# Performance work log

Measured on AMD Instinct MI355X. Metric: run time of the kernel, lower is better.

## Reference

```python
import jax, jax.numpy as jnp
import numpy as np

B = 1024
FEATS = [("sirna_gibbs_energy", 19), ("pssm_score", 1), ("gc_sterch", 1), ("sirna_second_percent", 2), ("sirna_second_energy", 2), ("tri_nt_percent", 64), ("di_nt_percent", 16), ("single_nt_percent", 4), ("gc_content", 1)]
DFF = 2048  # torch TransformerEncoderLayer default dim_feedforward


def _posenc(S, d):
    pos = jnp.arange(S, dtype=jnp.float32)[:, None]
    div = jnp.exp(jnp.arange(0, d, 2, dtype=jnp.float32) * (-np.log(10000.0) / d))
    pe = jnp.zeros((S, d), jnp.float32)
    pe = pe.at[:, 0::2].set(jnp.sin(pos * div))
    pe = pe.at[:, 1::2].set(jnp.cos(pos * div))
    return pe


def _ln(x, g, b):
    m = x.mean(-1, keepdims=True)
    v = ((x - m) ** 2).mean(-1, keepdims=True)
    return (x - m) * jax.lax.rsqrt(v + 1e-5) * g + b


def _encoder_layer(x, qkv_w, qkv_b, ow, ob, f1w, f1b, f2w, f2b, g1, b1, g2, b2, nhead):
    Bx, S, d = x.shape
    dh = d // nhead
    qkv = jnp.einsum('bsd,ed->bse', x, qkv_w) + qkv_b  # [B,S,3d]
    q, k, v = jnp.split(qkv, 3, axis=-1)
    sh = lambda t: t.reshape(Bx, S, nhead, dh).transpose(0, 2, 1, 3)  # [B,h,S,dh]
    q, k, v = sh(q), sh(k), sh(v)
    att = jax.nn.softmax(jnp.einsum('bhqd,bhkd->bhqk', q, k) / np.sqrt(dh).astype(np.float32), axis=-1)
    o = jnp.einsum('bhqk,bhkd->bhqd', att, v).transpose(0, 2, 1, 3).reshape(Bx, S, d)
    o = o @ ow.T + ob
    x = _ln(x + o, g1, b1)  # post-norm (norm_first=False default)
    h = jax.nn.relu(x @ f1w.T + f1b) @ f2w.T + f2b
    return _ln(x + h, g2, b2)


def _encoder(x, qkv_w, qkv_b, ow, ob, f1w, f1b, f2w, f2b, g1, b1, g2, b2, nhead):
    for i in range(qkv_w.shape[0]):
        x = _encoder_layer(x, qkv_w[i], qkv_b[i], ow[i], ob[i], f1w[i], f1b[i], f2w[i], f2b[i], g1[i], b1[i], g2[i], b2[i], nhead)
    return x


def setup_inputs():
    key = jax.random.key(0)
    ks = iter(jax.random.split(key, 128))
    inp = {}
    inp['rnafm_encode'] = jax.random.normal(next(ks), (B, 21, 640), jnp.float32)
    inp['rnafm_encode_mrna'] = jax.random.normal(next(ks), (B, 59, 640), jnp.float32)
    for name, n in FEATS:
        inp[name] = jax.random.normal(next(ks), (B, n, 1), jnp.float32)

    def xav(shape):
        fan_out, fan_in = shape[-2], shape[-1]
        std = np.sqrt(2.0 / (fan_in + fan_out)).astype(np.float32)
        return jax.random.normal(next(ks), shape, jnp.float32) * std

    def enc_params(prefix, L, d):
        inp[prefix + '_qkv_w'] = xav((L, 3 * d, d))
        inp[prefix + '_qkv_b'] = jnp.zeros((L, 3 * d), jnp.float32)
        inp[prefix + '_ow'] = xav((L, d, d))
        inp[prefix + '_ob'] = jnp.zeros((L, d), jnp.float32)
        inp[prefix + '_f1w'] = xav((L, DFF, d))
        inp[prefix + '_f1b'] = jnp.zeros((L, DFF), jnp.float32)
        inp[prefix + '_f2w'] = xav((L, d, DFF))
        inp[prefix + '_f2b'] = jnp.zeros((L, d), jnp.float32)
        inp[prefix + '_g1'] = jnp.ones((L, d), jnp.float32)
        inp[prefix + '_b1'] = jnp.zeros((L, d), jnp.float32)
        inp[prefix + '_g2'] = jnp.ones((L, d), jnp.float32)
        inp[prefix + '_b2'] = jnp.zeros((L, d), jnp.float32)

    inp['xmap1_w'] = xav((16, 640)); inp['xmap1_b'] = jnp.zeros(16, jnp.float32)
    enc_params('enc1', 4, 16)
    inp['ymap1_w'] = xav((4, 16)); inp['ymap1_b'] = jnp.zeros(4, jnp.float32)
    inp['xmap2_w'] = xav((8, 640)); inp['xmap2_b'] = jnp.zeros(8, jnp.float32)
    enc_params('enc2', 2, 8)
    inp['ymap2_w'] = xav((1, 8)); inp['ymap2_b'] = jnp.zeros(1, jnp.float32)
    inp['bn_g'] = jnp.ones(253, jnp.float32); inp['bn_b'] = jnp.zeros(253, jnp.float32)
    inp['d1w'] = xav((256, 253)); inp['d1b'] = jnp.zeros(256, jnp.float32)
    inp['d2w'] = xav((64, 256)); inp['d2b'] = jnp.zeros(64, jnp.float32)
    inp['d3w'] = xav((16, 64)); inp['d3b'] = jnp.zeros(16, jnp.float32)
    inp['d4w'] = xav((1, 16)); inp['d4b'] = jnp.zeros(1, jnp.float32)
    return inp


def _forward(rnafm_encode, rnafm_encode_mrna, feats,
             xmap1_w, xmap1_b, enc1, ymap1_w, ymap1_b,
             xmap2_w, xmap2_b, enc2, ymap2_w, ymap2_b,
             bn_g, bn_b, d1w, d1b, d2w, d2b, d3w, d3b, d4w, d4b):
    # siRNA branch: [B,21,640] -> [B,21,16] -> encoder(4 layers, 2 heads) -> [B,21,4]
    x = rnafm_encode @ xmap1_w.T + xmap1_b
    x = x + _posenc(21, 16)
    x = _encoder(x, *enc1, nhead=2)
    as_att = (x @ ymap1_w.T + ymap1_b).reshape(x.shape[0], -1)  # [B,84]
    # mRNA branch: [B,59,640] -> [B,59,8] -> encoder(2 layers, 1 head) -> [B,59,1]
    y = rnafm_encode_mrna @ xmap2_w.T + xmap2_b
    y = y + _posenc(59, 8)
    y = _encoder(y, *enc2, nhead=1)
    mrna_att = (y @ ymap2_w.T + ymap2_b).reshape(y.shape[0], -1)  # [B,59]
    other = jnp.concatenate([f[..., 0] for f in feats], axis=1)  # [B,110]
    cat = jnp.concatenate([as_att, mrna_att, other], axis=1)  # [B,253]
    # BatchNorm1d in eval mode (running_mean=0, running_var=1, eps=1e-5)
    h = cat * jax.lax.rsqrt(jnp.float32(1.0 + 1e-5)) * bn_g + bn_b
    h = jax.nn.leaky_relu(h @ d1w.T + d1b, 0.01)
    h = jax.nn.leaky_relu(h @ d2w.T + d2b, 0.01)
    h = jax.nn.leaky_relu(h @ d3w.T + d3b, 0.01)
    out = jax.nn.sigmoid(h @ d4w.T + d4b)
    return out[:, 0]


def reference(rnafm_encode, rnafm_encode_mrna, sirna_gibbs_energy, pssm_score, gc_sterch,
              sirna_second_percent, sirna_second_energy, tri_nt_percent, di_nt_percent,
              single_nt_percent, gc_content,
              xmap1_w, xmap1_b,
              enc1_qkv_w, enc1_qkv_b, enc1_ow, enc1_ob, enc1_f1w, enc1_f1b, enc1_f2w, enc1_f2b,
              enc1_g1, enc1_b1, enc1_g2, enc1_b2,
              ymap1_w, ymap1_b,
              xmap2_w, xmap2_b,
              enc2_qkv_w, enc2_qkv_b, enc2_ow, enc2_ob, enc2_f1w, enc2_f1b, enc2_f2w, enc2_f2b,
              enc2_g1, enc2_b1, enc2_g2, enc2_b2,
              ymap2_w, ymap2_b,
              bn_g, bn_b, d1w, d1b, d2w, d2b, d3w, d3b, d4w, d4b):
    feats = (sirna_gibbs_energy, pssm_score, gc_sterch, sirna_second_percent,
             sirna_second_energy, tri_nt_percent, di_nt_percent, single_nt_percent, gc_content)
    enc1 = (enc1_qkv_w, enc1_qkv_b, enc1_ow, enc1_ob, enc1_f1w, enc1_f1b, enc1_f2w, enc1_f2b,
            enc1_g1, enc1_b1, enc1_g2, enc1_b2)
    enc2 = (enc2_qkv_w, enc2_qkv_b, enc2_ow, enc2_ob, enc2_f1w, enc2_f1b, enc2_f2w, enc2_f2b,
            enc2_g1, enc2_b1, enc2_g2, enc2_b2)
    return _forward(rnafm_encode, rnafm_encode_mrna, feats,
                    xmap1_w, xmap1_b, enc1, ymap1_w, ymap1_b,
                    xmap2_w, xmap2_b, enc2, ymap2_w, ymap2_b,
                    bn_g, bn_b, d1w, d1b, d2w, d2b, d3w, d3b, d4w, d4b)
```

## Files before the change

kernel.cpp:

```cpp
#include <hip/hip_runtime.h>
#include <math.h>

#define NB 1024

typedef __bf16 mbf8 __attribute__((ext_vector_type(8)));
typedef float  mf4  __attribute__((ext_vector_type(4)));

union Pk { __bf16 h[4]; uint2 u2; };

__device__ __forceinline__ mf4 mfma16(mbf8 a, mbf8 b, mf4 c) {
  return __builtin_amdgcn_mfma_f32_16x16x32_bf16(a, b, c, 0, 0, 0);
}

__device__ __forceinline__ float dot4f(float4 a, float4 b){
  return a.x*b.x + a.y*b.y + a.z*b.z + a.w*b.w;
}

__global__ __launch_bounds__(256) void prep_kernel(
    const float* __restrict__ xw1, const float* __restrict__ f1w1, const float* __restrict__ f2w1,
    const float* __restrict__ xw2, const float* __restrict__ f1w2, const float* __restrict__ f2w2,
    __bf16* __restrict__ out)
{
  int idx = blockIdx.x * 256 + threadIdx.x;
  if (idx >= 610304) return;
  int which, local;
  if (idx < 10240)       { which = 0; local = idx; }
  else if (idx < 272384) { which = 1; local = idx - 10240; }
  else if (idx < 403456) { which = 2; local = idx - 272384; }
  else if (idx < 413696) { which = 3; local = idx - 403456; }
  else if (idx < 544768) { which = 4; local = idx - 413696; }
  else                   { which = 5; local = idx - 544768; }
  int tile = local >> 9, r = local & 511, lane = r >> 3, j = r & 7;
  int quad = lane >> 4, lm = lane & 15, khi = quad * 8 + j;
  float val = 0.f;
  switch (which) {
    case 0: { int k = tile*32 + khi; val = xw1[lm*640 + k]; } break;
    case 1: { int L = tile >> 7, nt = tile & 127, n = nt*16 + lm;
              val = (khi < 16) ? f1w1[(L*2048 + n)*16 + khi] : 0.f; } break;
    case 2: { int L = tile >> 6, ks = tile & 63, k = ks*32 + khi;
              val = f2w1[(L*16 + lm)*2048 + k]; } break;
    case 3: { int k = tile*32 + khi; val = (lm < 8) ? xw2[lm*640 + k] : 0.f; } break;
    case 4: { int L = tile >> 7, nt = tile & 127, n = nt*16 + lm;
              val = (khi < 8) ? f1w2[(L*2048 + n)*8 + khi] : 0.f; } break;
    default:{ int L = tile >> 6, ks = tile & 63, k = ks*32 + khi;
              val = (lm < 8) ? f2w2[(L*8 + lm)*2048 + k] : 0.f; } break;
  }
  out[idx] = (__bf16)val;
}

__global__ __launch_bounds__(256) void b1_kernel(
    const float* __restrict__ inp,
    const float* __restrict__ xb,
    const float* __restrict__ qw, const float* __restrict__ qb,
    const float* __restrict__ ow, const float* __restrict__ ob,
    const float* __restrict__ f1b, const float* __restrict__ f2b,
    const float* __restrict__ g1w, const float* __restrict__ b1w,
    const float* __restrict__ g2w, const float* __restrict__ b2w,
    const float* __restrict__ ymw, const float* __restrict__ ymb,
    const __bf16* __restrict__ xwB, const __bf16* __restrict__ w1B,
    const __bf16* __restrict__ w2B,
    float* __restrict__ outp)
{
  __shared__ __align__(16) float xs[21*20];
  __shared__ __align__(16) float xr[21*20];
  __shared__ __align__(16) float ao[21*20];
  __shared__ __align__(16) float pool[2176];
  __shared__ __align__(16) __bf16 hbuf[32*264];
  __shared__ float mu[21], rsd[21];

  const int tid = threadIdx.x;
  const int b = blockIdx.x;
  const int w = tid >> 6, lane = tid & 63, quad = lane >> 4, lm = lane & 15;
  float* qkv = pool;
  float* sc  = pool + 1092;
  float* red = pool;
  const float* Ain = inp + (size_t)b * 21 * 640;

  mf4 pc0 = {0.f,0.f,0.f,0.f}, pc1 = {0.f,0.f,0.f,0.f};
  for (int i = 0; i < 5; ++i) {
    int ks = w*5 + i;
    mbf8 bv = *(const mbf8*)(xwB + (ks*64 + lane)*8);
    #pragma unroll
    for (int mt = 0; mt < 2; ++mt) {
      int row = mt*16 + lm; row = row > 20 ? 20 : row;
      const float* src = Ain + row*640 + ks*32 + quad*8;
      float4 u0 = *(const float4*)src;
      float4 u1 = *(const float4*)(src + 4);
      mbf8 av;
      av[0]=(__bf16)u0.x; av[1]=(__bf16)u0.y; av[2]=(__bf16)u0.z; av[3]=(__bf16)u0.w;
      av[4]=(__bf16)u1.x; av[5]=(__bf16)u1.y; av[6]=(__bf16)u1.z; av[7]=(__bf16)u1.w;
      if (mt == 0) pc0 = mfma16(av, bv, pc0); else pc1 = mfma16(av, bv, pc1);
    }
  }
  #pragma unroll
  for (int r = 0; r < 4; ++r) {
    red[((w*2+0)*16 + quad*4 + r)*17 + lm] = pc0[r];
    red[((w*2+1)*16 + quad*4 + r)*17 + lm] = pc1[r];
  }
  __syncthreads();
  {
    const float lf = -logf(10000.0f) / 16.0f;
    for (int idx = tid; idx < 336; idx += 256) {
      int t = idx >> 4, i = idx & 15, mt = t >> 4, tl = t & 15;
      float s = red[((0+mt)*16+tl)*17+i] + red[((2+mt)*16+tl)*17+i]
              + red[((4+mt)*16+tl)*17+i] + red[((6+mt)*16+tl)*17+i];
      float freq = expf((float)((i>>1)*2) * lf);
      float pe = (i & 1) ? cosf((float)t * freq) : sinf((float)t * freq);
      xs[t*20 + i] = s + xb[i] + pe;
    }
  }
  __syncthreads();

  for (int L = 0; L < 4; ++L) {
    for (int idx = tid; idx < 1008; idx += 256) {
      int s = idx / 48, e = idx % 48;
      const float* wr = qw + (L*48 + e)*16;
      float a = qb[L*48 + e];
      #pragma unroll
      for (int k = 0; k < 16; ++k) a += xs[s*20+k] * wr[k];
      qkv[s*52 + e] = a;
    }
    __syncthreads();

    for (int idx = tid; idx < 882; idx += 256) {
      int h = idx / 441, r2 = idx % 441, i = r2 / 21, j = r2 % 21;
      float4 q0 = *(const float4*)(qkv + i*52 + h*8);
      float4 q1 = *(const float4*)(qkv + i*52 + h*8 + 4);
      float4 k0 = *(const float4*)(qkv + j*52 + 16 + h*8);
      float4 k1 = *(const float4*)(qkv + j*52 + 16 + h*8 + 4);
      sc[(h*21 + i)*23 + j] = (dot4f(q0,k0) + dot4f(q1,k1)) * 0.35355339059327373f;
    }
    __syncthreads();

    for (int r = tid; r < 42; r += 256) {
      float* row = sc + r*23;
      float m = row[0];
      for (int j = 1; j < 21; ++j) m = fmaxf(m, row[j]);
      float ssum = 0.f;
      for (int j = 0; j < 21; ++j) { float e = __expf(row[j] - m); row[j] = e; ssum += e; }
      float inv = 1.f / ssum;
      for (int j = 0; j < 21; ++j) row[j] *= inv;
    }
    __syncthreads();

    for (int idx = tid; idx < 336; idx += 256) {
      int s = idx >> 4, cc = idx & 15, h = cc >> 3, c = cc & 7;
      const float* row = sc + (h*21 + s)*23;
      float a = 0.f;
      for (int j = 0; j < 21; ++j) a += row[j] * qkv[j*52 + 32 + h*8 + c];
      ao[s*20 + cc] = a;
    }
    __syncthreads();

    for (int idx = tid; idx < 336; idx += 256) {
      int s = idx >> 4, i = idx & 15;
      const float* wr = ow + (L*16 + i)*16;
      float a = ob[L*16 + i];
      #pragma unroll
      for (int c = 0; c < 16; ++c) a += ao[s*20 + c] * wr[c];
      xr[s*20 + i] = xs[s*20 + i] + a;
    }
    __syncthreads();

    if (tid < 21) {
      float m = 0.f;
      #pragma unroll
      for (int k = 0; k < 16; ++k) m += xr[tid*20 + k];
      m *= (1.f/16.f);
      float v = 0.f;
      #pragma unroll
      for (int k = 0; k < 16; ++k) { float d = xr[tid*20 + k] - m; v += d*d; }
      v *= (1.f/16.f);
      mu[tid] = m; rsd[tid] = rsqrtf(v + 1e-5f);
    }
    __syncthreads();
    for (int idx = tid; idx < 336; idx += 256) {
      int s = idx >> 4, i = idx & 15;
      xs[s*20 + i] = (xr[s*20 + i] - mu[s]) * rsd[s] * g1w[L*16+i] + b1w[L*16+i];
    }
    __syncthreads();

    mbf8 xf0, xf1;
    {
      #pragma unroll
      for (int q = 0; q < 8; ++q) { xf0[q] = (__bf16)0.f; xf1[q] = (__bf16)0.f; }
      if (quad < 2) {
        int t0 = lm;
        int t1 = 16 + lm; if (t1 > 20) t1 = 20;
        const float* s0 = xs + t0*20 + quad*8;
        const float* s1 = xs + t1*20 + quad*8;
        float4 a0 = *(const float4*)s0, a1 = *(const float4*)(s0+4);
        float4 b0 = *(const float4*)s1, b1_ = *(const float4*)(s1+4);
        xf0[0]=(__bf16)a0.x; xf0[1]=(__bf16)a0.y; xf0[2]=(__bf16)a0.z; xf0[3]=(__bf16)a0.w;
        xf0[4]=(__bf16)a1.x; xf0[5]=(__bf16)a1.y; xf0[6]=(__bf16)a1.z; xf0[7]=(__bf16)a1.w;
        xf1[0]=(__bf16)b0.x; xf1[1]=(__bf16)b0.y; xf1[2]=(__bf16)b0.z; xf1[3]=(__bf16)b0.w;
        xf1[4]=(__bf16)b1_.x; xf1[5]=(__bf16)b1_.y; xf1[6]=(__bf16)b1_.z; xf1[7]=(__bf16)b1_.w;
      }
    }
    mf4 of0 = {0.f,0.f,0.f,0.f}, of1 = {0.f,0.f,0.f,0.f};
    const __bf16* w1L = w1B + (size_t)L*128*512;
    const __bf16* w2L = w2B + (size_t)L*64*512;
    const float* f1bL = f1b + L*2048;
    for (int ci = 0; ci < 8; ++ci) {
      #pragma unroll
      for (int u = 0; u < 4; ++u) {
        int ut = ci*16 + w*4 + u;
        mbf8 wa = *(const mbf8*)(w1L + (ut*64 + lane)*8);
        float4 bia = *(const float4*)(f1bL + ut*16 + quad*4);
        mf4 z = {0.f,0.f,0.f,0.f};
        mf4 c0 = mfma16(wa, xf0, z);
        mf4 c1 = mfma16(wa, xf1, z);
        Pk p0, p1;
        p0.h[0]=(__bf16)fmaxf(c0[0]+bia.x,0.f); p0.h[1]=(__bf16)fmaxf(c0[1]+bia.y,0.f);
        p0.h[2]=(__bf16)fmaxf(c0[2]+bia.z,0.f); p0.h[3]=(__bf16)fmaxf(c0[3]+bia.w,0.f);
        p1.h[0]=(__bf16)fmaxf(c1[0]+bia.x,0.f); p1.h[1]=(__bf16)fmaxf(c1[1]+bia.y,0.f);
        p1.h[2]=(__bf16)fmaxf(c1[2]+bia.z,0.f); p1.h[3]=(__bf16)fmaxf(c1[3]+bia.w,0.f);
        int colb = (ut & 15)*16 + quad*4;
        *(uint2*)(hbuf + lm*264 + colb)        = p0.u2;
        *(uint2*)(hbuf + (16 + lm)*264 + colb) = p1.u2;
      }
      #pragma unroll
      for (int kk = 0; kk < 2; ++kk) {
        int ksl = w*2 + kk;
        mbf8 wb = *(const mbf8*)(w2L + ((ci*8 + ksl)*64 + lane)*8);
        mbf8 a0 = *(const mbf8*)(hbuf + lm*264 + ksl*32 + quad*8);
        mbf8 a1 = *(const mbf8*)(hbuf + (16 + lm)*264 + ksl*32 + quad*8);
        of0 = mfma16(a0, wb, of0);
        of1 = mfma16(a1, wb, of1);
      }
    }
    __syncthreads();
    #pragma unroll
    for (int r = 0; r < 4; ++r) {
      red[((w*2+0)*16 + quad*4 + r)*17 + lm] = of0[r];
      red[((w*2+1)*16 + quad*4 + r)*17 + lm] = of1[r];
    }
    __syncthreads();
    for (int idx = tid; idx < 336; idx += 256) {
      int t = idx >> 4, i = idx & 15, mt = t >> 4, tl = t & 15;
      float s = red[((0+mt)*16+tl)*17+i] + red[((2+mt)*16+tl)*17+i]
              + red[((4+mt)*16+tl)*17+i] + red[((6+mt)*16+tl)*17+i];
      xr[t*20 + i] = xs[t*20 + i] + s + f2b[L*16 + i];
    }
    __syncthreads();
    if (tid < 21) {
      float m = 0.f;
      #pragma unroll
      for (int k = 0; k < 16; ++k) m += xr[tid*20 + k];
      m *= (1.f/16.f);
      float v = 0.f;
      #pragma unroll
      for (int k = 0; k < 16; ++k) { float d = xr[tid*20 + k] - m; v += d*d; }
      v *= (1.f/16.f);
      mu[tid] = m; rsd[tid] = rsqrtf(v + 1e-5f);
    }
    __syncthreads();
    for (int idx = tid; idx < 336; idx += 256) {
      int s = idx >> 4, i = idx & 15;
      xs[s*20 + i] = (xr[s*20 + i] - mu[s]) * rsd[s] * g2w[L*16+i] + b2w[L*16+i];
    }
    __syncthreads();
  }

  for (int idx = tid; idx < 84; idx += 256) {
    int s = idx >> 2, j = idx & 3;
    float a = ymb[j];
    #pragma unroll
    for (int k = 0; k < 16; ++k) a += xs[s*20 + k] * ymw[j*16 + k];
    outp[(size_t)b*84 + idx] = a;
  }
}

__global__ __launch_bounds__(256) void b2_kernel(
    const float* __restrict__ inp,
    const float* __restrict__ xb,
    const float* __restrict__ qw, const float* __restrict__ qb,
    const float* __restrict__ ow, const float* __restrict__ ob,
    const float* __restrict__ f1b, const float* __restrict__ f2b,
    const float* __restrict__ g1w, const float* __restrict__ b1w,
    const float* __restrict__ g2w, const float* __restrict__ b2w,
    const float* __restrict__ ymw, const float* __restrict__ ymb,
    const __bf16* __restrict__ xwB, const __bf16* __restrict__ w1B,
    const __bf16* __restrict__ w2B,
    float* __restrict__ outp)
{
  __shared__ __align__(16) float xs[59*12];
  __shared__ __align__(16) float xr[59*12];
  __shared__ __align__(16) float ao[59*12];
  __shared__ __align__(16) float pool[5251];
  __shared__ __align__(16) __bf16 hbuf[64*136];
  __shared__ float mu[59], rsd[59];

  const int tid = threadIdx.x;
  const int b = blockIdx.x;
  const int w = tid >> 6, lane = tid & 63, quad = lane >> 4, lm = lane & 15;
  float* qkv = pool;
  float* sc  = pool + 1652;
  float* red = pool;
  const float* Ain = inp + (size_t)b * 59 * 640;

  mf4 pc[4];
  #pragma unroll
  for (int mt = 0; mt < 4; ++mt) { mf4 z = {0.f,0.f,0.f,0.f}; pc[mt] = z; }
  for (int i = 0; i < 5; ++i) {
    int ks = w*5 + i;
    mbf8 bv = *(const mbf8*)(xwB + (ks*64 + lane)*8);
    #pragma unroll
    for (int mt = 0; mt < 4; ++mt) {
      int row = mt*16 + lm; row = row > 58 ? 58 : row;
      const float* src = Ain + row*640 + ks*32 + quad*8;
      float4 u0 = *(const float4*)src;
      float4 u1 = *(const float4*)(src + 4);
      mbf8 av;
      av[0]=(__bf16)u0.x; av[1]=(__bf16)u0.y; av[2]=(__bf16)u0.z; av[3]=(__bf16)u0.w;
      av[4]=(__bf16)u1.x; av[5]=(__bf16)u1.y; av[6]=(__bf16)u1.z; av[7]=(__bf16)u1.w;
      pc[mt] = mfma16(av, bv, pc[mt]);
    }
  }
  #pragma unroll
  for (int mt = 0; mt < 4; ++mt)
    #pragma unroll
    for (int r = 0; r < 4; ++r)
      red[((w*4+mt)*16 + quad*4 + r)*17 + lm] = pc[mt][r];
  __syncthreads();
  {
    const float lf = -logf(10000.0f) / 8.0f;
    for (int idx = tid; idx < 472; idx += 256) {
      int t = idx >> 3, i = idx & 7, mt = t >> 4, tl = t & 15;
      float s = red[((0*4+mt)*16+tl)*17+i] + red[((1*4+mt)*16+tl)*17+i]
              + red[((2*4+mt)*16+tl)*17+i] + red[((3*4+mt)*16+tl)*17+i];
      float freq = expf((float)((i>>1)*2) * lf);
      float pe = (i & 1) ? cosf((float)t * freq) : sinf((float)t * freq);
      xs[t*12 + i] = s + xb[i] + pe;
    }
  }
  __syncthreads();

  for (int L = 0; L < 2; ++L) {
    for (int idx = tid; idx < 1416; idx += 256) {
      int s = idx / 24, e = idx % 24;
      const float* wr = qw + (L*24 + e)*8;
      float a = qb[L*24 + e];
      #pragma unroll
      for (int k = 0; k < 8; ++k) a += xs[s*12+k] * wr[k];
      qkv[s*28 + e] = a;
    }
    __syncthreads();

    for (int idx = tid; idx < 3481; idx += 256) {
      int i = idx / 59, j = idx % 59;
      float4 q0 = *(const float4*)(qkv + i*28);
      float4 q1 = *(const float4*)(qkv + i*28 + 4);
      float4 k0 = *(const float4*)(qkv + j*28 + 8);
      float4 k1 = *(const float4*)(qkv + j*28 + 12);
      sc[i*61 + j] = (dot4f(q0,k0) + dot4f(q1,k1)) * 0.35355339059327373f;
    }
    __syncthreads();

    for (int r = tid; r < 59; r += 256) {
      float* row = sc + r*61;
      float m = row[0];
      for (int j = 1; j < 59; ++j) m = fmaxf(m, row[j]);
      float ssum = 0.f;
      for (int j = 0; j < 59; ++j) { float e = __expf(row[j] - m); row[j] = e; ssum += e; }
      float inv = 1.f / ssum;
      for (int j = 0; j < 59; ++j) row[j] *= inv;
    }
    __syncthreads();

    for (int idx = tid; idx < 472; idx += 256) {
      int s = idx >> 3, c = idx & 7;
      const float* row = sc + s*61;
      float a = 0.f;
      for (int j = 0; j < 59; ++j) a += row[j] * qkv[j*28 + 16 + c];
      ao[s*12 + c] = a;
    }
    __syncthreads();

    for (int idx = tid; idx < 472; idx += 256) {
      int s = idx >> 3, i = idx & 7;
      const float* wr = ow + (L*8 + i)*8;
      float a = ob[L*8 + i];
      #pragma unroll
      for (int c = 0; c < 8; ++c) a += ao[s*12 + c] * wr[c];
      xr[s*12 + i] = xs[s*12 + i] + a;
    }
    __syncthreads();

    if (tid < 59) {
      float m = 0.f;
      #pragma unroll
      for (int k = 0; k < 8; ++k) m += xr[tid*12 + k];
      m *= 0.125f;
      float v = 0.f;
      #pragma unroll
      for (int k = 0; k < 8; ++k) { float d = xr[tid*12 + k] - m; v += d*d; }
      v *= 0.125f;
      mu[tid] = m; rsd[tid] = rsqrtf(v + 1e-5f);
    }
    __syncthreads();
    for (int idx = tid; idx < 472; idx += 256) {
      int s = idx >> 3, i = idx & 7;
      xs[s*12 + i] = (xr[s*12 + i] - mu[s]) * rsd[s] * g1w[L*8+i] + b1w[L*8+i];
    }
    __syncthreads();

    mbf8 xf[4];
    #pragma unroll
    for (int tt = 0; tt < 4; ++tt) {
      #pragma unroll
      for (int q = 0; q < 8; ++q) xf[tt][q] = (__bf16)0.f;
      if (quad == 0) {
        int tok = tt*16 + lm; if (tok > 58) tok = 58;
        const float* src = xs + tok*12;
        float4 u0 = *(const float4*)src, u1 = *(const float4*)(src + 4);
        xf[tt][0]=(__bf16)u0.x; xf[tt][1]=(__bf16)u0.y; xf[tt][2]=(__bf16)u0.z; xf[tt][3]=(__bf16)u0.w;
        xf[tt][4]=(__bf16)u1.x; xf[tt][5]=(__bf16)u1.y; xf[tt][6]=(__bf16)u1.z; xf[tt][7]=(__bf16)u1.w;
      }
    }
    mf4 of[4];
    #pragma unroll
    for (int mt = 0; mt < 4; ++mt) { mf4 z = {0.f,0.f,0.f,0.f}; of[mt] = z; }
    const __bf16* w1L = w1B + (size_t)L*128*512;
    const __bf16* w2L = w2B + (size_t)L*64*512;
    const float* f1bL = f1b + L*2048;
    for (int ci = 0; ci < 16; ++ci) {
      #pragma unroll
      for (int u = 0; u < 2; ++u) {
        int ut = ci*8 + w*2 + u;
        mbf8 wa = *(const mbf8*)(w1L + (ut*64 + lane)*8);
        float4 bia = *(const float4*)(f1bL + ut*16 + quad*4);
        int colb = (ut & 7)*16 + quad*4;
        #pragma unroll
        for (int tt = 0; tt < 4; ++tt) {
          mf4 z = {0.f,0.f,0.f,0.f};
          mf4 c = mfma16(wa, xf[tt], z);
          Pk p;
          p.h[0]=(__bf16)fmaxf(c[0]+bia.x,0.f); p.h[1]=(__bf16)fmaxf(c[1]+bia.y,0.f);
          p.h[2]=(__bf16)fmaxf(c[2]+bia.z,0.f); p.h[3]=(__bf16)fmaxf(c[3]+bia.w,0.f);
          *(uint2*)(hbuf + (tt*16 + lm)*136 + colb) = p.u2;
        }
      }
      {
        mbf8 wb = *(const mbf8*)(w2L + ((ci*4 + w)*64 + lane)*8);
        #pragma unroll
        for (int mt = 0; mt < 4; ++mt) {
          mbf8 ah = *(const mbf8*)(hbuf + (mt*16 + lm)*136 + w*32 + quad*8);
          of[mt] = mfma16(ah, wb, of[mt]);
        }
      }
    }
    __syncthreads();
    #pragma unroll
    for (int mt = 0; mt < 4; ++mt)
      #pragma unroll
      for (int r = 0; r < 4; ++r)
        red[((w*4+mt)*16 + quad*4 + r)*17 + lm] = of[mt][r];
    __syncthreads();
    for (int idx = tid; idx < 472; idx += 256) {
      int t = idx >> 3, i = idx & 7, mt = t >> 4, tl = t & 15;
      float s = red[((0*4+mt)*16+tl)*17+i] + red[((1*4+mt)*16+tl)*17+i]
              + red[((2*4+mt)*16+tl)*17+i] + red[((3*4+mt)*16+tl)*17+i];
      xr[t*12 + i] = xs[t*12 + i] + s + f2b[L*8 + i];
    }
    __syncthreads();
    if (tid < 59) {
      float m = 0.f;
      #pragma unroll
      for (int k = 0; k < 8; ++k) m += xr[tid*12 + k];
      m *= 0.125f;
      float v = 0.f;
      #pragma unroll
      for (int k = 0; k < 8; ++k) { float d = xr[tid*12 + k] - m; v += d*d; }
      v *= 0.125f;
      mu[tid] = m; rsd[tid] = rsqrtf(v + 1e-5f);
    }
    __syncthreads();
    for (int idx = tid; idx < 472; idx += 256) {
      int s = idx >> 3, i = idx & 7;
      xs[s*12 + i] = (xr[s*12 + i] - mu[s]) * rsd[s] * g2w[L*8+i] + b2w[L*8+i];
    }
    __syncthreads();
  }

  for (int s = tid; s < 59; s += 256) {
    float a = ymb[0];
    #pragma unroll
    for (int k = 0; k < 8; ++k) a += xs[s*12 + k] * ymw[k];
    outp[(size_t)b*59 + s] = a;
  }
}

__global__ __launch_bounds__(256) void mlp_kernel(
    const float* __restrict__ as_att, const float* __restrict__ mrna,
    const float* __restrict__ f_gibbs, const float* __restrict__ f_pssm,
    const float* __restrict__ f_gcs, const float* __restrict__ f_ssp,
    const float* __restrict__ f_sse, const float* __restrict__ f_tri,
    const float* __restrict__ f_di, const float* __restrict__ f_sgl,
    const float* __restrict__ f_gc,
    const float* __restrict__ bn_g, const float* __restrict__ bn_b,
    const float* __restrict__ d1w, const float* __restrict__ d1b,
    const float* __restrict__ d2w, const float* __restrict__ d2b,
    const float* __restrict__ d3w, const float* __restrict__ d3b,
    const float* __restrict__ d4w, const float* __restrict__ d4b,
    float* __restrict__ outp)
{
  __shared__ float cat[256];
  __shared__ float l1[256];
  __shared__ float l2[64];
  __shared__ float l3[16];
  const int tid = threadIdx.x;
  const int b   = blockIdx.x;
  const float bnscale = rsqrtf(1.0f + 1e-5f);

  if (tid < 253) {
    float v;
    if (tid < 84)       v = as_att[(size_t)b*84 + tid];
    else if (tid < 143) v = mrna[(size_t)b*59 + (tid - 84)];
    else {
      int j = tid - 143;
      if (j < 19)       v = f_gibbs[b*19 + j];
      else if (j < 20)  v = f_pssm[b];
      else if (j < 21)  v = f_gcs[b];
      else if (j < 23)  v = f_ssp[b*2 + (j-21)];
      else if (j < 25)  v = f_sse[b*2 + (j-23)];
      else if (j < 89)  v = f_tri[b*64 + (j-25)];
      else if (j < 105) v = f_di[b*16 + (j-89)];
      else if (j < 109) v = f_sgl[b*4 + (j-105)];
      else              v = f_gc[b];
    }
    cat[tid] = v * bnscale * bn_g[tid] + bn_b[tid];
  }
  __syncthreads();

  {
    float a = d1b[tid];
    const float* w = d1w + (size_t)tid * 253;
    for (int j = 0; j < 253; ++j) a += cat[j] * w[j];
    l1[tid] = (a > 0.f) ? a : 0.01f * a;
  }
  __syncthreads();
  if (tid < 64) {
    float a = d2b[tid];
    const float* w = d2w + (size_t)tid * 256;
    for (int j = 0; j < 256; ++j) a += l1[j] * w[j];
    l2[tid] = (a > 0.f) ? a : 0.01f * a;
  }
  __syncthreads();
  if (tid < 16) {
    float a = d3b[tid];
    const float* w = d3w + tid * 64;
    for (int j = 0; j < 64; ++j) a += l2[j] * w[j];
    l3[tid] = (a > 0.f) ? a : 0.01f * a;
  }
  __syncthreads();
  if (tid == 0) {
    float a = d4b[0];
    #pragma unroll
    for (int j = 0; j < 16; ++j) a += l3[j] * d4w[j];
    outp[b] = 1.f / (1.f + __expf(-a));
  }
}

extern "C" void kernel_launch(void* const* d_in, const int* in_sizes, int n_in,
                              void* d_out, int out_size, void* d_ws, size_t ws_size,
                              hipStream_t stream) {
  const float* rnafm   = (const float*)d_in[0];
  const float* rnafm_m = (const float*)d_in[1];
  const float* f_gibbs = (const float*)d_in[2];
  const float* f_pssm  = (const float*)d_in[3];
  const float* f_gcs   = (const float*)d_in[4];
  const float* f_ssp   = (const float*)d_in[5];
  const float* f_sse   = (const float*)d_in[6];
  const float* f_tri   = (const float*)d_in[7];
  const float* f_di    = (const float*)d_in[8];
  const float* f_sgl   = (const float*)d_in[9];
  const float* f_gc    = (const float*)d_in[10];
  const float* xmap1_w = (const float*)d_in[11];
  const float* xmap1_b = (const float*)d_in[12];
  const float* e1_qw   = (const float*)d_in[13];
  const float* e1_qb   = (const float*)d_in[14];
  const float* e1_ow   = (const float*)d_in[15];
  const float* e1_ob   = (const float*)d_in[16];
  const float* e1_f1w  = (const float*)d_in[17];
  const float* e1_f1b  = (const float*)d_in[18];
  const float* e1_f2w  = (const float*)d_in[19];
  const float* e1_f2b  = (const float*)d_in[20];
  const float* e1_g1   = (const float*)d_in[21];
  const float* e1_b1   = (const float*)d_in[22];
  const float* e1_g2   = (const float*)d_in[23];
  const float* e1_b2   = (const float*)d_in[24];
  const float* ymap1_w = (const float*)d_in[25];
  const float* ymap1_b = (const float*)d_in[26];
  const float* xmap2_w = (const float*)d_in[27];
  const float* xmap2_b = (const float*)d_in[28];
  const float* e2_qw   = (const float*)d_in[29];
  const float* e2_qb   = (const float*)d_in[30];
  const float* e2_ow   = (const float*)d_in[31];
  const float* e2_ob   = (const float*)d_in[32];
  const float* e2_f1w  = (const float*)d_in[33];
  const float* e2_f1b  = (const float*)d_in[34];
  const float* e2_f2w  = (const float*)d_in[35];
  const float* e2_f2b  = (const float*)d_in[36];
  const float* e2_g1   = (const float*)d_in[37];
  const float* e2_b1   = (const float*)d_in[38];
  const float* e2_g2   = (const float*)d_in[39];
  const float* e2_b2   = (const float*)d_in[40];
  const float* ymap2_w = (const float*)d_in[41];
  const float* ymap2_b = (const float*)d_in[42];
  const float* bn_g    = (const float*)d_in[43];
  const float* bn_b    = (const float*)d_in[44];
  const float* d1w     = (const float*)d_in[45];
  const float* d1b     = (const float*)d_in[46];
  const float* d2w     = (const float*)d_in[47];
  const float* d2b     = (const float*)d_in[48];
  const float* d3w     = (const float*)d_in[49];
  const float* d3b     = (const float*)d_in[50];
  const float* d4w     = (const float*)d_in[51];
  const float* d4b     = (const float*)d_in[52];

  float* as_att = (float*)d_ws;
  float* mrna   = (float*)((char*)d_ws + (size_t)NB*84*4);
  __bf16* bfb   = (__bf16*)((char*)d_ws + 585728);
  __bf16* xw1B  = bfb;
  __bf16* w1B1  = bfb + 10240;
  __bf16* w2B1  = bfb + 272384;
  __bf16* xw2B  = bfb + 403456;
  __bf16* w1B2  = bfb + 413696;
  __bf16* w2B2  = bfb + 544768;
  float* outp   = (float*)d_out;

  prep_kernel<<<2384, 256, 0, stream>>>(xmap1_w, e1_f1w, e1_f2w, xmap2_w, e2_f1w, e2_f2w, bfb);

  b1_kernel<<<NB, 256, 0, stream>>>(rnafm, xmap1_b,
      e1_qw, e1_qb, e1_ow, e1_ob, e1_f1b, e1_f2b,
      e1_g1, e1_b1, e1_g2, e1_b2, ymap1_w, ymap1_b,
      xw1B, w1B1, w2B1, as_att);

  b2_kernel<<<NB, 256, 0, stream>>>(rnafm_m, xmap2_b,
      e2_qw, e2_qb, e2_ow, e2_ob, e2_f1b, e2_f2b,
      e2_g1, e2_b1, e2_g2, e2_b2, ymap2_w, ymap2_b,
      xw2B, w1B2, w2B2, mrna);

  mlp_kernel<<<NB, 256, 0, stream>>>(as_att, mrna,
      f_gibbs, f_pssm, f_gcs, f_ssp, f_sse, f_tri, f_di, f_sgl, f_gc,
      bn_g, bn_b, d1w, d1b, d2w, d2b, d3w, d3b, d4w, d4b, outp);
}
```

Baseline: 573.9 us.

## Batch MLP head on MFMA, alias hbuf into pool, parallelize softmax

The MLP head now processes 16 samples per block and runs its three dense layers with bf16 MFMA instructions. The weights for those layers are converted by the prep kernel into fragment layout, replacing the per-sample scalar fp32 dot products. The encoder kernels alias the FFN hidden buffer into the shared pool to cut LDS use and pad its row stride. Softmax rows are now split across 4 lanes with shuffle reductions instead of one thread per row. This adds bf16 rounding in the MLP head, and the head launches only 64 blocks, which limits its parallelism.

```diff
diff --git a/kernel.cpp b/kernel.cpp
--- a/kernel.cpp
+++ b/kernel.cpp
@@ -16,20 +16,33 @@
   return a.x*b.x + a.y*b.y + a.z*b.z + a.w*b.w;
 }
 
+__device__ __forceinline__ mbf8 ld_frag_f32(const float* p) {
+  float4 u0 = *(const float4*)p;
+  float4 u1 = *(const float4*)(p + 4);
+  mbf8 v;
+  v[0]=(__bf16)u0.x; v[1]=(__bf16)u0.y; v[2]=(__bf16)u0.z; v[3]=(__bf16)u0.w;
+  v[4]=(__bf16)u1.x; v[5]=(__bf16)u1.y; v[6]=(__bf16)u1.z; v[7]=(__bf16)u1.w;
+  return v;
+}
+
 __global__ __launch_bounds__(256) void prep_kernel(
     const float* __restrict__ xw1, const float* __restrict__ f1w1, const float* __restrict__ f2w1,
     const float* __restrict__ xw2, const float* __restrict__ f1w2, const float* __restrict__ f2w2,
+    const float* __restrict__ d1w, const float* __restrict__ d2w, const float* __restrict__ d3w,
     __bf16* __restrict__ out)
 {
   int idx = blockIdx.x * 256 + threadIdx.x;
-  if (idx >= 610304) return;
+  if (idx >= 693248) return;
   int which, local;
   if (idx < 10240)       { which = 0; local = idx; }
   else if (idx < 272384) { which = 1; local = idx - 10240; }
   else if (idx < 403456) { which = 2; local = idx - 272384; }
   else if (idx < 413696) { which = 3; local = idx - 403456; }
   else if (idx < 544768) { which = 4; local = idx - 413696; }
-  else                   { which = 5; local = idx - 544768; }
+  else if (idx < 610304) { which = 5; local = idx - 544768; }
+  else if (idx < 675840) { which = 6; local = idx - 610304; }
+  else if (idx < 692224) { which = 7; local = idx - 675840; }
+  else                   { which = 8; local = idx - 692224; }
   int tile = local >> 9, r = local & 511, lane = r >> 3, j = r & 7;
   int quad = lane >> 4, lm = lane & 15, khi = quad * 8 + j;
   float val = 0.f;
@@ -42,8 +55,14 @@
     case 3: { int k = tile*32 + khi; val = (lm < 8) ? xw2[lm*640 + k] : 0.f; } break;
     case 4: { int L = tile >> 7, nt = tile & 127, n = nt*16 + lm;
               val = (khi < 8) ? f1w2[(L*2048 + n)*8 + khi] : 0.f; } break;
-    default:{ int L = tile >> 6, ks = tile & 63, k = ks*32 + khi;
+    case 5: { int L = tile >> 6, ks = tile & 63, k = ks*32 + khi;
               val = (lm < 8) ? f2w2[(L*8 + lm)*2048 + k] : 0.f; } break;
+    case 6: { int nt = tile >> 3, ks = tile & 7, k = ks*32 + khi;
+              val = (k < 253) ? d1w[(nt*16 + lm)*253 + k] : 0.f; } break;
+    case 7: { int nt = tile >> 3, ks = tile & 7, k = ks*32 + khi;
+              val = d2w[(nt*16 + lm)*256 + k]; } break;
+    default:{ int ks = tile, k = ks*32 + khi;
+              val = d3w[lm*64 + k]; } break;
   }
   out[idx] = (__bf16)val;
 }
@@ -64,8 +83,7 @@
   __shared__ __align__(16) float xs[21*20];
   __shared__ __align__(16) float xr[21*20];
   __shared__ __align__(16) float ao[21*20];
-  __shared__ __align__(16) float pool[2176];
-  __shared__ __align__(16) __bf16 hbuf[32*264];
+  __shared__ __align__(16) float pool[4288];
   __shared__ float mu[21], rsd[21];
 
   const int tid = threadIdx.x;
@@ -74,6 +92,7 @@
   float* qkv = pool;
   float* sc  = pool + 1092;
   float* red = pool;
+  __bf16* hbuf = (__bf16*)pool;
   const float* Ain = inp + (size_t)b * 21 * 640;
 
   mf4 pc0 = {0.f,0.f,0.f,0.f}, pc1 = {0.f,0.f,0.f,0.f};
@@ -83,12 +102,7 @@
     #pragma unroll
     for (int mt = 0; mt < 2; ++mt) {
       int row = mt*16 + lm; row = row > 20 ? 20 : row;
-      const float* src = Ain + row*640 + ks*32 + quad*8;
-      float4 u0 = *(const float4*)src;
-      float4 u1 = *(const float4*)(src + 4);
-      mbf8 av;
-      av[0]=(__bf16)u0.x; av[1]=(__bf16)u0.y; av[2]=(__bf16)u0.z; av[3]=(__bf16)u0.w;
-      av[4]=(__bf16)u1.x; av[5]=(__bf16)u1.y; av[6]=(__bf16)u1.z; av[7]=(__bf16)u1.w;
+      mbf8 av = ld_frag_f32(Ain + row*640 + ks*32 + quad*8);
       if (mt == 0) pc0 = mfma16(av, bv, pc0); else pc1 = mfma16(av, bv, pc1);
     }
   }
@@ -132,14 +146,21 @@
     }
     __syncthreads();
 
-    for (int r = tid; r < 42; r += 256) {
-      float* row = sc + r*23;
-      float m = row[0];
-      for (int j = 1; j < 21; ++j) m = fmaxf(m, row[j]);
-      float ssum = 0.f;
-      for (int j = 0; j < 21; ++j) { float e = __expf(row[j] - m); row[j] = e; ssum += e; }
-      float inv = 1.f / ssum;
-      for (int j = 0; j < 21; ++j) row[j] *= inv;
+    {
+      int r = tid >> 2, p = tid & 3;
+      if (r < 42) {
+        float* row = sc + r*23;
+        float m = -1e30f;
+        for (int j = p; j < 21; j += 4) m = fmaxf(m, row[j]);
+        m = fmaxf(m, __shfl_xor(m, 1));
+        m = fmaxf(m, __shfl_xor(m, 2));
+        float ssum = 0.f;
+        for (int j = p; j < 21; j += 4) { float e = __expf(row[j] - m); row[j] = e; ssum += e; }
+        ssum += __shfl_xor(ssum, 1);
+        ssum += __shfl_xor(ssum, 2);
+        float inv = 1.f / ssum;
+        for (int j = p; j < 21; j += 4) row[j] *= inv;
+      }
     }
     __syncthreads();
 
@@ -187,14 +208,8 @@
       if (quad < 2) {
         int t0 = lm;
         int t1 = 16 + lm; if (t1 > 20) t1 = 20;
-        const float* s0 = xs + t0*20 + quad*8;
-        const float* s1 = xs + t1*20 + quad*8;
-        float4 a0 = *(const float4*)s0, a1 = *(const float4*)(s0+4);
-        float4 b0 = *(const float4*)s1, b1_ = *(const float4*)(s1+4);
-        xf0[0]=(__bf16)a0.x; xf0[1]=(__bf16)a0.y; xf0[2]=(__bf16)a0.z; xf0[3]=(__bf16)a0.w;
-        xf0[4]=(__bf16)a1.x; xf0[5]=(__bf16)a1.y; xf0[6]=(__bf16)a1.z; xf0[7]=(__bf16)a1.w;
-        xf1[0]=(__bf16)b0.x; xf1[1]=(__bf16)b0.y; xf1[2]=(__bf16)b0.z; xf1[3]=(__bf16)b0.w;
-        xf1[4]=(__bf16)b1_.x; xf1[5]=(__bf16)b1_.y; xf1[6]=(__bf16)b1_.z; xf1[7]=(__bf16)b1_.w;
+        xf0 = ld_frag_f32(xs + t0*20 + quad*8);
+        xf1 = ld_frag_f32(xs + t1*20 + quad*8);
       }
     }
     mf4 of0 = {0.f,0.f,0.f,0.f}, of1 = {0.f,0.f,0.f,0.f};
@@ -216,15 +231,15 @@
         p1.h[0]=(__bf16)fmaxf(c1[0]+bia.x,0.f); p1.h[1]=(__bf16)fmaxf(c1[1]+bia.y,0.f);
         p1.h[2]=(__bf16)fmaxf(c1[2]+bia.z,0.f); p1.h[3]=(__bf16)fmaxf(c1[3]+bia.w,0.f);
         int colb = (ut & 15)*16 + quad*4;
-        *(uint2*)(hbuf + lm*264 + colb)        = p0.u2;
-        *(uint2*)(hbuf + (16 + lm)*264 + colb) = p1.u2;
+        *(uint2*)(hbuf + lm*268 + colb)        = p0.u2;
+        *(uint2*)(hbuf + (16 + lm)*268 + colb) = p1.u2;
       }
       #pragma unroll
       for (int kk = 0; kk < 2; ++kk) {
         int ksl = w*2 + kk;
         mbf8 wb = *(const mbf8*)(w2L + ((ci*8 + ksl)*64 + lane)*8);
-        mbf8 a0 = *(const mbf8*)(hbuf + lm*264 + ksl*32 + quad*8);
-        mbf8 a1 = *(const mbf8*)(hbuf + (16 + lm)*264 + ksl*32 + quad*8);
+        mbf8 a0 = *(const mbf8*)(hbuf + lm*268 + ksl*32 + quad*8);
+        mbf8 a1 = *(const mbf8*)(hbuf + (16 + lm)*268 + ksl*32 + quad*8);
         of0 = mfma16(a0, wb, of0);
         of1 = mfma16(a1, wb, of1);
       }
@@ -288,7 +303,6 @@
   __shared__ __align__(16) float xr[59*12];
   __shared__ __align__(16) float ao[59*12];
   __shared__ __align__(16) float pool[5251];
-  __shared__ __align__(16) __bf16 hbuf[64*136];
   __shared__ float mu[59], rsd[59];
 
   const int tid = threadIdx.x;
@@ -297,6 +311,7 @@
   float* qkv = pool;
   float* sc  = pool + 1652;
   float* red = pool;
+  __bf16* hbuf = (__bf16*)pool;
   const float* Ain = inp + (size_t)b * 59 * 640;
 
   mf4 pc[4];
@@ -308,12 +323,7 @@
     #pragma unroll
     for (int mt = 0; mt < 4; ++mt) {
       int row = mt*16 + lm; row = row > 58 ? 58 : row;
-      const float* src = Ain + row*640 + ks*32 + quad*8;
-      float4 u0 = *(const float4*)src;
-      float4 u1 = *(const float4*)(src + 4);
-      mbf8 av;
-      av[0]=(__bf16)u0.x; av[1]=(__bf16)u0.y; av[2]=(__bf16)u0.z; av[3]=(__bf16)u0.w;
-      av[4]=(__bf16)u1.x; av[5]=(__bf16)u1.y; av[6]=(__bf16)u1.z; av[7]=(__bf16)u1.w;
+      mbf8 av = ld_frag_f32(Ain + row*640 + ks*32 + quad*8);
       pc[mt] = mfma16(av, bv, pc[mt]);
     }
   }
@@ -357,14 +367,21 @@
     }
     __syncthreads();
 
-    for (int r = tid; r < 59; r += 256) {
-      float* row = sc + r*61;
-      float m = row[0];
-      for (int j = 1; j < 59; ++j) m = fmaxf(m, row[j]);
-      float ssum = 0.f;
-      for (int j = 0; j < 59; ++j) { float e = __expf(row[j] - m); row[j] = e; ssum += e; }
-      float inv = 1.f / ssum;
-      for (int j = 0; j < 59; ++j) row[j] *= inv;
+    {
+      int r = tid >> 2, p = tid & 3;
+      if (r < 59) {
+        float* row = sc + r*61;
+        float m = -1e30f;
+        for (int j = p; j < 59; j += 4) m = fmaxf(m, row[j]);
+        m = fmaxf(m, __shfl_xor(m, 1));
+        m = fmaxf(m, __shfl_xor(m, 2));
+        float ssum = 0.f;
+        for (int j = p; j < 59; j += 4) { float e = __expf(row[j] - m); row[j] = e; ssum += e; }
+        ssum += __shfl_xor(ssum, 1);
+        ssum += __shfl_xor(ssum, 2);
+        float inv = 1.f / ssum;
+        for (int j = p; j < 59; j += 4) row[j] *= inv;
+      }
     }
     __syncthreads();
 
@@ -412,10 +429,7 @@
       for (int q = 0; q < 8; ++q) xf[tt][q] = (__bf16)0.f;
       if (quad == 0) {
         int tok = tt*16 + lm; if (tok > 58) tok = 58;
-        const float* src = xs + tok*12;
-        float4 u0 = *(const float4*)src, u1 = *(const float4*)(src + 4);
-        xf[tt][0]=(__bf16)u0.x; xf[tt][1]=(__bf16)u0.y; xf[tt][2]=(__bf16)u0.z; xf[tt][3]=(__bf16)u0.w;
-        xf[tt][4]=(__bf16)u1.x; xf[tt][5]=(__bf16)u1.y; xf[tt][6]=(__bf16)u1.z; xf[tt][7]=(__bf16)u1.w;
+        xf[tt] = ld_frag_f32(xs + tok*12);
       }
     }
     mf4 of[4];
@@ -438,14 +452,14 @@
           Pk p;
           p.h[0]=(__bf16)fmaxf(c[0]+bia.x,0.f); p.h[1]=(__bf16)fmaxf(c[1]+bia.y,0.f);
           p.h[2]=(__bf16)fmaxf(c[2]+bia.z,0.f); p.h[3]=(__bf16)fmaxf(c[3]+bia.w,0.f);
-          *(uint2*)(hbuf + (tt*16 + lm)*136 + colb) = p.u2;
+          *(uint2*)(hbuf + (tt*16 + lm)*140 + colb) = p.u2;
         }
       }
       {
         mbf8 wb = *(const mbf8*)(w2L + ((ci*4 + w)*64 + lane)*8);
         #pragma unroll
         for (int mt = 0; mt < 4; ++mt) {
-          mbf8 ah = *(const mbf8*)(hbuf + (mt*16 + lm)*136 + w*32 + quad*8);
+          mbf8 ah = *(const mbf8*)(hbuf + (mt*16 + lm)*140 + w*32 + quad*8);
           of[mt] = mfma16(ah, wb, of[mt]);
         }
       }
@@ -499,66 +513,111 @@
     const float* __restrict__ f_di, const float* __restrict__ f_sgl,
     const float* __restrict__ f_gc,
     const float* __restrict__ bn_g, const float* __restrict__ bn_b,
-    const float* __restrict__ d1w, const float* __restrict__ d1b,
-    const float* __restrict__ d2w, const float* __restrict__ d2b,
-    const float* __restrict__ d3w, const float* __restrict__ d3b,
+    const float* __restrict__ d1b, const float* __restrict__ d2b,
+    const float* __restrict__ d3b,
     const float* __restrict__ d4w, const float* __restrict__ d4b,
+    const __bf16* __restrict__ d1B, const __bf16* __restrict__ d2B,
+    const __bf16* __restrict__ d3B,
     float* __restrict__ outp)
 {
-  __shared__ float cat[256];
-  __shared__ float l1[256];
-  __shared__ float l2[64];
-  __shared__ float l3[16];
+  __shared__ __align__(16) float cat[16*268];
+  __shared__ __align__(16) float h1[16*268];
+  __shared__ __align__(16) float h2[16*68];
+  __shared__ __align__(16) float h3[16*17];
   const int tid = threadIdx.x;
-  const int b   = blockIdx.x;
+  const int bs  = blockIdx.x * 16;
+  const int w = tid >> 6, lane = tid & 63, quad = lane >> 4, lm = lane & 15;
   const float bnscale = rsqrtf(1.0f + 1e-5f);
 
-  if (tid < 253) {
-    float v;
-    if (tid < 84)       v = as_att[(size_t)b*84 + tid];
-    else if (tid < 143) v = mrna[(size_t)b*59 + (tid - 84)];
-    else {
-      int j = tid - 143;
-      if (j < 19)       v = f_gibbs[b*19 + j];
-      else if (j < 20)  v = f_pssm[b];
-      else if (j < 21)  v = f_gcs[b];
-      else if (j < 23)  v = f_ssp[b*2 + (j-21)];
-      else if (j < 25)  v = f_sse[b*2 + (j-23)];
-      else if (j < 89)  v = f_tri[b*64 + (j-25)];
-      else if (j < 105) v = f_di[b*16 + (j-89)];
-      else if (j < 109) v = f_sgl[b*4 + (j-105)];
-      else              v = f_gc[b];
-    }
-    cat[tid] = v * bnscale * bn_g[tid] + bn_b[tid];
-  }
+  for (int g = 0; g < 16; ++g) {
+    int smp = bs + g;
+    for (int j = tid; j < 253; j += 256) {
+      float v;
+      if (j < 84)       v = as_att[(size_t)smp*84 + j];
+      else if (j < 143) v = mrna[(size_t)smp*59 + (j - 84)];
+      else {
+        int j2 = j - 143;
+        if (j2 < 19)       v = f_gibbs[smp*19 + j2];
+        else if (j2 < 20)  v = f_pssm[smp];
+        else if (j2 < 21)  v = f_gcs[smp];
+        else if (j2 < 23)  v = f_ssp[smp*2 + (j2-21)];
+        else if (j2 < 25)  v = f_sse[smp*2 + (j2-23)];
+        else if (j2 < 89)  v = f_tri[smp*64 + (j2-25)];
+        else if (j2 < 105) v = f_di[smp*16 + (j2-89)];
+        else if (j2 < 109) v = f_sgl[smp*4 + (j2-105)];
+        else               v = f_gc[smp];
+      }
+      cat[g*268 + j] = v * bnscale * bn_g[j] + bn_b[j];
+    }
+  }
+  if (tid < 48) { int g = tid / 3; cat[g*268 + 253 + tid % 3] = 0.f; }
   __syncthreads();
 
   {
-    float a = d1b[tid];
-    const float* w = d1w + (size_t)tid * 253;
-    for (int j = 0; j < 253; ++j) a += cat[j] * w[j];
-    l1[tid] = (a > 0.f) ? a : 0.01f * a;
+    mf4 acc[4];
+    #pragma unroll
+    for (int q = 0; q < 4; ++q) { mf4 z = {0.f,0.f,0.f,0.f}; acc[q] = z; }
+    for (int ks = 0; ks < 8; ++ks) {
+      mbf8 af = ld_frag_f32(cat + lm*268 + ks*32 + quad*8);
+      #pragma unroll
+      for (int nt4 = 0; nt4 < 4; ++nt4) {
+        int nt = w*4 + nt4;
+        mbf8 bf = *(const mbf8*)(d1B + ((nt*8 + ks)*64 + lane)*8);
+        acc[nt4] = mfma16(af, bf, acc[nt4]);
+      }
+    }
+    #pragma unroll
+    for (int nt4 = 0; nt4 < 4; ++nt4) {
+      int n = (w*4 + nt4)*16 + lm;
+      float bb = d1b[n];
+      #pragma unroll
+      for (int r = 0; r < 4; ++r) {
+        float a = acc[nt4][r] + bb;
+        h1[(quad*4 + r)*268 + n] = (a > 0.f) ? a : 0.01f * a;
+      }
+    }
   }
   __syncthreads();
-  if (tid < 64) {
-    float a = d2b[tid];
-    const float* w = d2w + (size_t)tid * 256;
-    for (int j = 0; j < 256; ++j) a += l1[j] * w[j];
-    l2[tid] = (a > 0.f) ? a : 0.01f * a;
+
+  {
+    mf4 acc = {0.f,0.f,0.f,0.f};
+    for (int ks = 0; ks < 8; ++ks) {
+      mbf8 af = ld_frag_f32(h1 + lm*268 + ks*32 + quad*8);
+      mbf8 bf = *(const mbf8*)(d2B + ((w*8 + ks)*64 + lane)*8);
+      acc = mfma16(af, bf, acc);
+    }
+    int n = w*16 + lm;
+    float bb = d2b[n];
+    #pragma unroll
+    for (int r = 0; r < 4; ++r) {
+      float a = acc[r] + bb;
+      h2[(quad*4 + r)*68 + n] = (a > 0.f) ? a : 0.01f * a;
+    }
   }
   __syncthreads();
+
+  if (w == 0) {
+    mf4 acc = {0.f,0.f,0.f,0.f};
+    #pragma unroll
+    for (int ks = 0; ks < 2; ++ks) {
+      mbf8 af = ld_frag_f32(h2 + lm*68 + ks*32 + quad*8);
+      mbf8 bf = *(const mbf8*)(d3B + (ks*64 + lane)*8);
+      acc = mfma16(af, bf, acc);
+    }
+    float bb = d3b[lm];
+    #pragma unroll
+    for (int r = 0; r < 4; ++r) {
+      float a = acc[r] + bb;
+      h3[(quad*4 + r)*17 + lm] = (a > 0.f) ? a : 0.01f * a;
+    }
+  }
+  __syncthreads();
+
   if (tid < 16) {
-    float a = d3b[tid];
-    const float* w = d3w + tid * 64;
-    for (int j = 0; j < 64; ++j) a += l2[j] * w[j];
-    l3[tid] = (a > 0.f) ? a : 0.01f * a;
-  }
-  __syncthreads();
-  if (tid == 0) {
     float a = d4b[0];
     #pragma unroll
-    for (int j = 0; j < 16; ++j) a += l3[j] * d4w[j];
-    outp[b] = 1.f / (1.f + __expf(-a));
+    for (int j = 0; j < 16; ++j) a += h3[tid*17 + j] * d4w[j];
+    outp[bs + tid] = 1.f / (1.f + __expf(-a));
   }
 }
 
@@ -628,9 +687,13 @@
   __bf16* xw2B  = bfb + 403456;
   __bf16* w1B2  = bfb + 413696;
   __bf16* w2B2  = bfb + 544768;
+  __bf16* d1B   = bfb + 610304;
+  __bf16* d2B   = bfb + 675840;
+  __bf16* d3B   = bfb + 692224;
   float* outp   = (float*)d_out;
 
-  prep_kernel<<<2384, 256, 0, stream>>>(xmap1_w, e1_f1w, e1_f2w, xmap2_w, e2_f1w, e2_f2w, bfb);
+  prep_kernel<<<2708, 256, 0, stream>>>(xmap1_w, e1_f1w, e1_f2w, xmap2_w, e2_f1w, e2_f2w,
+                                        d1w, d2w, d3w, bfb);
 
   b1_kernel<<<NB, 256, 0, stream>>>(rnafm, xmap1_b,
       e1_qw, e1_qb, e1_ow, e1_ob, e1_f1b, e1_f2b,
@@ -642,7 +705,7 @@
       e2_g1, e2_b1, e2_g2, e2_b2, ymap2_w, ymap2_b,
       xw2B, w1B2, w2B2, mrna);
 
-  mlp_kernel<<<NB, 256, 0, stream>>>(as_att, mrna,
+  mlp_kernel<<<64, 256, 0, stream>>>(as_att, mrna,
       f_gibbs, f_pssm, f_gcs, f_ssp, f_sse, f_tri, f_di, f_sgl, f_gc,
-      bn_g, bn_b, d1w, d1b, d2w, d2b, d3w, d3b, d4w, d4b, outp);
+      bn_g, bn_b, d1b, d2b, d3b, d4w, d4b, d1B, d2B, d3B, outp);
 }
```

After: 574.3 us. Within noise of the previous version (+0.1%).
